# Optimization experiments

Measured on AMD Instinct MI355X. Metric: run time of the kernel, lower is better.

The kernel has to match this reference:

```python
import jax, jax.numpy as jnp
import numpy as np
from jax import lax

NPOINTS = [1024, 256, 64, 16]
RADII = [0.02, 0.04, 0.06, 0.08]
NSAMPLE = [32, 32, 16, 16]
# per-level MLP widths; first entry already includes the +3 for use_xyz concat
MLPS = [[6, 32, 32, 64], [67, 64, 64, 128], [131, 128, 128, 256], [259, 256, 256, 512]]
EPS = 1e-5


def setup_inputs() -> dict:
    key = jax.random.key(0)
    B, N = 8, 16384
    pc = jax.random.uniform(jax.random.fold_in(key, 0), (B, N, 6), jnp.float32)
    # xyz into a 0.2-cube so the hard-coded radii (0.02..0.08) find real neighborhoods
    pc = pc.at[..., :3].multiply(0.2)
    inp = {"pointcloud": pc}
    ki = 1
    for l, m in enumerate(MLPS):
        for j in range(len(m) - 1):
            cin, cout = m[j], m[j + 1]
            inp[f"w{l}{j}"] = jax.random.normal(jax.random.fold_in(key, ki), (cin, cout), jnp.float32) * (1.0 / float(np.sqrt(cin)))
            inp[f"g{l}{j}"] = jnp.ones((cout,), jnp.float32)
            inp[f"b{l}{j}"] = jnp.zeros((cout,), jnp.float32)
            ki += 1
    return inp


def _fps(xyz, npoint):
    # iterative farthest point sampling, start at index 0 (matches CUDA kernel)
    B, N, _ = xyz.shape

    def step(carry, _):
        mind, last = carry
        lastp = jnp.take_along_axis(xyz, last[:, None, None], axis=1)  # [B,1,3]
        d = jnp.sum((xyz - lastp) ** 2, axis=-1)                       # [B,N]
        mind = jnp.minimum(mind, d)
        nxt = jnp.argmax(mind, axis=1).astype(jnp.int32)
        return (mind, nxt), last

    init = (jnp.full((B, N), 1e10, xyz.dtype), jnp.zeros((B,), jnp.int32))
    _, idx = lax.scan(step, init, None, length=npoint)
    return jnp.transpose(idx)  # [B,npoint]


def _gather(pts, idx):
    # pts [B,N,C], idx [B,...] -> [B,...,C]
    return jax.vmap(lambda p, i: p[i])(pts, idx)


def _ball_query(xyz, centers, radius, nsample):
    # first nsample points (in index order) within radius; pad with first hit (0 if none)
    N = xyz.shape[1]
    d2 = jnp.sum((centers[:, :, None, :] - xyz[:, None, :, :]) ** 2, axis=-1)  # [B,S,N]
    key = jnp.where(d2 < radius * radius, jnp.arange(N, dtype=jnp.int32), N)
    negtop, _ = lax.top_k(-key, nsample)
    sel = -negtop                      # ascending candidate indices
    valid = sel < N
    first = jnp.where(valid[..., :1], sel[..., :1], 0)
    return jnp.where(valid, sel, first)  # [B,S,nsample] int32


def _sa(xyz, feats, npoint, radius, nsample, layers):
    fps_idx = lax.stop_gradient(_fps(xyz, npoint))
    new_xyz = _gather(xyz, fps_idx)                    # [B,S,3]
    idx = _ball_query(xyz, new_xyz, radius, nsample)   # [B,S,K]
    g = _gather(xyz, idx) - new_xyz[:, :, None, :]     # centered grouped xyz [B,S,K,3]
    g = jnp.concatenate([g, _gather(feats, idx)], axis=-1)  # use_xyz concat -> [B,S,K,3+C]
    x = g
    for W, gamma, beta in layers:
        x = jnp.einsum('bski,io->bsko', x, W)          # 1x1 conv, bias=False (bn on)
        mu = jnp.mean(x, axis=(0, 1, 2))               # BN training-mode batch stats
        var = jnp.var(x, axis=(0, 1, 2))
        x = jax.nn.relu(gamma * (x - mu) * lax.rsqrt(var + EPS) + beta)
    return new_xyz, jnp.max(x, axis=2)                 # max-pool over neighbors -> [B,S,Cout]


def reference(pointcloud, w00, g00, b00, w01, g01, b01, w02, g02, b02,
              w10, g10, b10, w11, g11, b11, w12, g12, b12,
              w20, g20, b20, w21, g21, b21, w22, g22, b22,
              w30, g30, b30, w31, g31, b31, w32, g32, b32):
    params = [
        [(w00, g00, b00), (w01, g01, b01), (w02, g02, b02)],
        [(w10, g10, b10), (w11, g11, b11), (w12, g12, b12)],
        [(w20, g20, b20), (w21, g21, b21), (w22, g22, b22)],
        [(w30, g30, b30), (w31, g31, b31), (w32, g32, b32)],
    ]
    xyz = pointcloud[..., :3]
    feats = pointcloud[..., 3:]   # channels-last (torch keeps [B,C,N]; pure layout diff)
    l_xyz, l_feats = [xyz], [feats]
    for k in range(4):
        nx, nf = _sa(l_xyz[k], l_feats[k], NPOINTS[k], RADII[k], NSAMPLE[k], params[k])
        l_xyz.append(nx)
        l_feats.append(nf)
    return tuple(l_xyz) + tuple(l_feats)
```

## Files before the change

kernel.cpp:

```cpp
#include <hip/hip_runtime.h>

#define WAVE 64

__global__ __launch_bounds__(256) void split_kernel(const float* __restrict__ pc,
    float* __restrict__ xyz, float* __restrict__ feats, int total) {
  int t = blockIdx.x * blockDim.x + threadIdx.x;
  if (t >= total) return;
  const float* p = pc + (size_t)t * 6;
  xyz[t * 3 + 0] = p[0]; xyz[t * 3 + 1] = p[1]; xyz[t * 3 + 2] = p[2];
  feats[t * 3 + 0] = p[3]; feats[t * 3 + 1] = p[4]; feats[t * 3 + 2] = p[5];
}

__global__ __launch_bounds__(256) void zero_kernel(float* __restrict__ p, int n) {
  int t = blockIdx.x * blockDim.x + threadIdx.x;
  if (t < n) p[t] = 0.f;
}

__device__ __forceinline__ float dpp_max_f32(float v) {
#define DPP_STEP_F(ctrl) { int t_ = __builtin_amdgcn_update_dpp( \
      __float_as_int(v), __float_as_int(v), ctrl, 0xf, 0xf, false); \
    v = fmaxf(v, __int_as_float(t_)); }
  DPP_STEP_F(0x111) DPP_STEP_F(0x112) DPP_STEP_F(0x114)
  DPP_STEP_F(0x118) DPP_STEP_F(0x142) DPP_STEP_F(0x143)
#undef DPP_STEP_F
  return v;
}
__device__ __forceinline__ unsigned dpp_max_u32(unsigned v) {
#define DPP_STEP_U(ctrl) { unsigned t_ = (unsigned)__builtin_amdgcn_update_dpp( \
      (int)v, (int)v, ctrl, 0xf, 0xf, false); \
    v = (t_ > v) ? t_ : v; }
  DPP_STEP_U(0x111) DPP_STEP_U(0x112) DPP_STEP_U(0x114)
  DPP_STEP_U(0x118) DPP_STEP_U(0x142) DPP_STEP_U(0x143)
#undef DPP_STEP_U
  return v;
}
__device__ __forceinline__ unsigned bcast63(unsigned v) {
  return (unsigned)__builtin_amdgcn_readlane((int)v, 63);
}

__global__ __launch_bounds__(1024, 4) void fps_big_kernel(const float* __restrict__ xyz,
    float* __restrict__ new_xyz, int N, int S) {
  const int b = blockIdx.x;
  const int tid = threadIdx.x;
  const int lane = tid & 63;
  const float* px = xyz + (size_t)b * N * 3;
  __shared__ unsigned long long s_key[3];
  float rx[16], ry[16], rz[16], mind[16];
#pragma unroll
  for (int p = 0; p < 16; ++p) {
    int i = tid + p * 1024;
    rx[p] = px[i * 3 + 0]; ry[p] = px[i * 3 + 1]; rz[p] = px[i * 3 + 2];
    asm volatile("" : "+v"(rx[p]), "+v"(ry[p]), "+v"(rz[p]));
    mind[p] = 1e10f;
  }
  if (tid < 3) s_key[tid] = 0ull;
  float qx = px[0], qy = px[1], qz = px[2];
  if (tid == 0) {
    float* o = new_xyz + (size_t)b * S * 3;
    o[0] = qx; o[1] = qy; o[2] = qz;
  }
  __syncthreads();
  for (unsigned it = 1; it < (unsigned)S; ++it) {
    float bestv = -1.f; unsigned besti = 0;
#pragma unroll
    for (int p = 0; p < 16; ++p) {
      float dx = __fsub_rn(rx[p], qx);
      float dy = __fsub_rn(ry[p], qy);
      float dz = __fsub_rn(rz[p], qz);
      float d = __fadd_rn(__fadd_rn(__fmul_rn(dx, dx), __fmul_rn(dy, dy)), __fmul_rn(dz, dz));
      float mo = fminf(mind[p], d);
      mind[p] = mo;
      if (mo > bestv) { bestv = mo; besti = (unsigned)(tid + p * 1024); }
    }
    float wm = dpp_max_f32(bestv);
    unsigned wmb = bcast63(__float_as_uint(wm));
    unsigned cand = (__float_as_uint(bestv) == wmb) ? (0xFFFFFFFFu - besti) : 0u;
    unsigned winv = bcast63(dpp_max_u32(cand));
    if (lane == 0) atomicMax(&s_key[it % 3u], ((unsigned long long)wmb << 32) | winv);
    if (tid == 0) s_key[(it + 1) % 3u] = 0ull;
    __syncthreads();
    unsigned long long k = s_key[it % 3u];
    int last = (int)(0xFFFFFFFFu - (unsigned)k);
    const float* q = px + (size_t)last * 3;
    qx = q[0]; qy = q[1]; qz = q[2];
    if (tid == 0) {
      float* o = new_xyz + ((size_t)b * S + it) * 3;
      o[0] = qx; o[1] = qy; o[2] = qz;
    }
  }
}

__global__ void fps_small_kernel(const float* __restrict__ xyz,
    float* __restrict__ new_xyz, int N, int S) {
  const int b = blockIdx.x;
  const int tid = threadIdx.x;
  const int lane = tid & 63;
  const float* px = xyz + (size_t)b * N * 3;
  __shared__ float sx[1024], sy[1024], sz[1024];
  __shared__ unsigned long long s_key[3];
  float x = px[tid * 3 + 0], y = px[tid * 3 + 1], z = px[tid * 3 + 2];
  sx[tid] = x; sy[tid] = y; sz[tid] = z;
  if (tid < 3) s_key[tid] = 0ull;
  float mind = 1e10f;
  float qx = px[0], qy = px[1], qz = px[2];
  if (tid == 0) {
    float* o = new_xyz + (size_t)b * S * 3;
    o[0] = qx; o[1] = qy; o[2] = qz;
  }
  __syncthreads();
  for (unsigned it = 1; it < (unsigned)S; ++it) {
    float dx = __fsub_rn(x, qx);
    float dy = __fsub_rn(y, qy);
    float dz = __fsub_rn(z, qz);
    float d = __fadd_rn(__fadd_rn(__fmul_rn(dx, dx), __fmul_rn(dy, dy)), __fmul_rn(dz, dz));
    mind = fminf(mind, d);
    float wm = dpp_max_f32(mind);
    unsigned wmb = bcast63(__float_as_uint(wm));
    unsigned cand = (__float_as_uint(mind) == wmb) ? (0xFFFFFFFFu - (unsigned)tid) : 0u;
    unsigned winv = bcast63(dpp_max_u32(cand));
    if (lane == 0) atomicMax(&s_key[it % 3u], ((unsigned long long)wmb << 32) | winv);
    if (tid == 0) s_key[(it + 1) % 3u] = 0ull;
    __syncthreads();
    unsigned long long k = s_key[it % 3u];
    int last = (int)(0xFFFFFFFFu - (unsigned)k);
    qx = sx[last]; qy = sy[last]; qz = sz[last];
    if (tid == 0) {
      float* o = new_xyz + ((size_t)b * S + it) * 3;
      o[0] = qx; o[1] = qy; o[2] = qz;
    }
  }
}

__global__ __launch_bounds__(256) void ballquery_kernel(const float* __restrict__ xyz,
    const float* __restrict__ centers, int* __restrict__ out_idx,
    int N, int S, int nsample, float r2) {
  int gw = (blockIdx.x * blockDim.x + threadIdx.x) >> 6;
  int lane = threadIdx.x & 63;
  int b = gw / S;
  int s = gw - b * S;
  const float* px = xyz + (size_t)b * N * 3;
  const float* cp = centers + ((size_t)b * S + s) * 3;
  float cx = cp[0], cy = cp[1], cz = cp[2];
  int* out = out_idx + ((size_t)b * S + s) * nsample;
  int cnt = 0;
  int firsti = 0;
  for (int base = 0; base < N; base += WAVE) {
    int i = base + lane;
    float dx = __fsub_rn(cx, px[i * 3 + 0]);
    float dy = __fsub_rn(cy, px[i * 3 + 1]);
    float dz = __fsub_rn(cz, px[i * 3 + 2]);
    float d = __fadd_rn(__fadd_rn(__fmul_rn(dx, dx), __fmul_rn(dy, dy)), __fmul_rn(dz, dz));
    bool hit = d < r2;
    unsigned long long m = __ballot(hit);
    if (hit) {
      int slot = cnt + __popcll(m & ((1ull << lane) - 1ull));
      if (slot < nsample) out[slot] = i;
    }
    if (cnt == 0 && m) firsti = base + __ffsll((unsigned long long)m) - 1;
    cnt += __popcll(m);
    if (cnt >= nsample) break;
  }
  for (int q = cnt + lane; q < nsample; q += WAVE) out[q] = firsti;
}

__global__ __launch_bounds__(256) void group_kernel(const float* __restrict__ xyz,
    const float* __restrict__ feats, const float* __restrict__ centers,
    const int* __restrict__ idx, float* __restrict__ X,
    int N, int S, int K, int ci, int R) {
  int t = blockIdx.x * blockDim.x + threadIdx.x;
  int C0 = ci + 3;
  int r = t / C0;
  if (r >= R) return;
  int c = t - r * C0;
  int g = r / K;
  int b = g / S;
  int j = idx[r];
  float v;
  if (c < 3) v = __fsub_rn(xyz[((size_t)b * N + j) * 3 + c], centers[(size_t)g * 3 + c]);
  else       v = feats[((size_t)b * N + j) * ci + (c - 3)];
  X[(size_t)r * C0 + c] = v;
}

#define BM 64
#define BN 64
#define BK 16
__global__ __launch_bounds__(256) void mm_fused_kernel(const float* __restrict__ A,
    const float* __restrict__ W, float* __restrict__ Y,
    float* __restrict__ st_out, const float* __restrict__ st_in,
    const float* __restrict__ g_in, const float* __restrict__ b_in,
    int R, int C, int Co, float inv_n) {
  __shared__ float As[BK][BM + 4];
  __shared__ float Bs[BK][BN + 4];
  __shared__ float s_mu[260], s_rs[260], s_g[260], s_b[260];
  __shared__ float s_sum[BN], s_sq[BN];
  int r0 = blockIdx.x * BM;
  int n0 = blockIdx.y * BN;
  int tid = threadIdx.x;
  int tx = tid & 15, ty = tid >> 4;
  if (st_in) {
    for (int c = tid; c < C; c += 256) {
      float mu = st_in[c] * inv_n;
      float var = st_in[512 + c] * inv_n - mu * mu;
      s_mu[c] = mu; s_rs[c] = rsqrtf(var + 1e-5f);
      s_g[c] = g_in[c]; s_b[c] = b_in[c];
    }
  }
  if (tid < BN) { s_sum[tid] = 0.f; s_sq[tid] = 0.f; }
  __syncthreads();
  float acc[4][4] = {};
  for (int k0 = 0; k0 < C; k0 += BK) {
#pragma unroll
    for (int u = 0; u < 4; ++u) {
      int lin = tid + u * 256;
      int row = lin >> 4;
      int cc = lin & 15;
      int c = k0 + cc;
      float v = 0.f;
      if (c < C) {
        v = A[(size_t)(r0 + row) * C + c];
        if (st_in) {
          v = s_g[c] * ((v - s_mu[c]) * s_rs[c]) + s_b[c];
          v = v > 0.f ? v : 0.f;
        }
      }
      As[cc][row] = v;
    }
#pragma unroll
    for (int u = 0; u < 4; ++u) {
      int lin = tid + u * 256;
      int kk = lin >> 6;
      int n = lin & 63;
      int c = k0 + kk;
      Bs[kk][n] = (c < C && (n0 + n) < Co) ? W[(size_t)c * Co + n0 + n] : 0.f;
    }
    __syncthreads();
#pragma unroll
    for (int kk = 0; kk < BK; ++kk) {
      float a0[4], b0[4];
#pragma unroll
      for (int i = 0; i < 4; ++i) a0[i] = As[kk][ty * 4 + i];
#pragma unroll
      for (int jj = 0; jj < 4; ++jj) b0[jj] = Bs[kk][tx * 4 + jj];
#pragma unroll
      for (int i = 0; i < 4; ++i)
#pragma unroll
        for (int jj = 0; jj < 4; ++jj)
          acc[i][jj] = fmaf(a0[i], b0[jj], acc[i][jj]);
    }
    __syncthreads();
  }
#pragma unroll
  for (int i = 0; i < 4; ++i) {
    int r = r0 + ty * 4 + i;
#pragma unroll
    for (int jj = 0; jj < 4; ++jj) {
      int n = n0 + tx * 4 + jj;
      if (n < Co) Y[(size_t)r * Co + n] = acc[i][jj];
    }
  }
#pragma unroll
  for (int jj = 0; jj < 4; ++jj) {
    float cs = 0.f, cq = 0.f;
#pragma unroll
    for (int i = 0; i < 4; ++i) { float v = acc[i][jj]; cs += v; cq += v * v; }
    atomicAdd(&s_sum[tx * 4 + jj], cs);
    atomicAdd(&s_sq[tx * 4 + jj], cq);
  }
  __syncthreads();
  if (tid < BN) {
    int n = n0 + tid;
    if (n < Co) {
      atomicAdd(&st_out[n], s_sum[tid]);
      atomicAdd(&st_out[512 + n], s_sq[tid]);
    }
  }
}

__global__ __launch_bounds__(256) void norm_relu_max_kernel(const float* __restrict__ Y,
    float* __restrict__ O, const float* __restrict__ st,
    const float* __restrict__ gamma, const float* __restrict__ beta,
    int G, int K, int Co, float inv_n) {
  int t = blockIdx.x * blockDim.x + threadIdx.x;
  if (t >= G * Co) return;
  int c = t & (Co - 1);
  int g = t / Co;
  float mu = st[c] * inv_n;
  float var = st[512 + c] * inv_n - mu * mu;
  float rs = rsqrtf(var + 1e-5f);
  float ga = gamma[c], be = beta[c];
  const float* yp = Y + (size_t)g * K * Co + c;
  float m = -1e30f;
  for (int k = 0; k < K; ++k) {
    float v = ga * ((yp[(size_t)k * Co] - mu) * rs) + be;
    m = fmaxf(m, v);
  }
  O[t] = m > 0.f ? m : 0.f;
}

extern "C" void kernel_launch(void* const* d_in, const int* in_sizes, int n_in,
                              void* d_out, int out_size, void* d_ws, size_t ws_size,
                              hipStream_t stream) {
  const float* pc = (const float*)d_in[0];
  float* out = (float*)d_out;
  char* wsb = (char*)d_ws;

  int* ballidx = (int*)wsb;
  float* stats = (float*)(wsb + ((size_t)1 << 20));
  float* bufA = (float*)(wsb + ((size_t)3 << 20));
  float* bufB = (float*)(wsb + ((size_t)37 << 20));

  const int B = 8;
  static const int Ns[4] = {16384, 1024, 256, 64};
  static const int Ss[4] = {1024, 256, 64, 16};
  static const int Ks[4] = {32, 32, 16, 16};
  static const double Rr[4] = {0.02, 0.04, 0.06, 0.08};
  static const int Ci[4] = {3, 64, 128, 256};
  static const int mlp[4][4] = {{6,32,32,64},{67,64,64,128},{131,128,128,256},{259,256,256,512}};
  static const size_t ox[5] = {0, 393216, 417792, 423936, 425472};
  static const size_t of[5] = {425856, 819072, 1343360, 1605504, 1736576};

  split_kernel<<<(B * 16384 + 255) / 256, 256, 0, stream>>>(pc, out + ox[0], out + of[0], B * 16384);
  zero_kernel<<<(12 * 1024 + 255) / 256, 256, 0, stream>>>(stats, 12 * 1024);

  for (int l = 0; l < 4; ++l) {
    const float* xyz = out + ox[l];
    const float* fts = out + of[l];
    float* nxyz = out + ox[l + 1];
    const int N = Ns[l], S = Ss[l], K = Ks[l], ci = Ci[l], C0 = ci + 3;
    const float r2 = (float)(Rr[l] * Rr[l]);

    if (l == 0) fps_big_kernel<<<B, 1024, 0, stream>>>(xyz, nxyz, N, S);
    else        fps_small_kernel<<<B, N, 0, stream>>>(xyz, nxyz, N, S);

    ballquery_kernel<<<(B * S) / 4, 256, 0, stream>>>(xyz, nxyz, ballidx, N, S, K, r2);

    const int R = B * S * K;
    {
      int total = R * C0;
      group_kernel<<<(total + 255) / 256, 256, 0, stream>>>(xyz, fts, nxyz, ballidx, bufA,
                                                            N, S, K, ci, R);
    }

    const float inv_n = 1.0f / (float)R;
    float* X = bufA; float* Y = bufB;
    const float* prev_st = nullptr;
    const float* prev_g = nullptr;
    const float* prev_b = nullptr;
    for (int j = 0; j < 3; ++j) {
      const int cin = mlp[l][j], cout = mlp[l][j + 1];
      const float* Wt = (const float*)d_in[1 + (l * 3 + j) * 3 + 0];
      const float* Ga = (const float*)d_in[1 + (l * 3 + j) * 3 + 1];
      const float* Be = (const float*)d_in[1 + (l * 3 + j) * 3 + 2];
      float* st = stats + (size_t)(l * 3 + j) * 1024;
      dim3 grid(R / 64, (cout + 63) / 64);
      mm_fused_kernel<<<grid, 256, 0, stream>>>(X, Wt, Y, st, prev_st, prev_g, prev_b,
                                                R, cin, cout, inv_n);
      if (j < 2) {
        prev_st = st; prev_g = Ga; prev_b = Be;
        float* tswap = X; X = Y; Y = tswap;
      } else {
        int G = B * S;
        int tot = G * cout;
        norm_relu_max_kernel<<<(tot + 255) / 256, 256, 0, stream>>>(Y, out + of[l + 1], st, Ga, Be,
                                                                    G, K, cout, inv_n);
      }
    }
  }
}
```

Baseline: 2.788 ms.

## Split level-0 farthest point sampling across eight cooperating blocks per batch

The single-block-per-batch FPS for the 16384-point level is replaced by eight blocks per batch, each owning a 2048-point chunk. Every iteration, each block publishes its local argmax key to a global slot array and spins on the other blocks' slots, with a timeout fallback. The aim is to cut the serial per-iteration distance work and raise GPU occupancy, at the cost of a cross-block global-memory handshake on every one of the 1024 iterations. The zero kernel is widened so it also clears the new slot region in the workspace. Correctness relies on all 64 blocks being co-resident.

```diff
diff --git a/kernel.cpp b/kernel.cpp
--- a/kernel.cpp
+++ b/kernel.cpp
@@ -38,39 +38,47 @@
   return (unsigned)__builtin_amdgcn_readlane((int)v, 63);
 }
 
-__global__ __launch_bounds__(1024, 4) void fps_big_kernel(const float* __restrict__ xyz,
-    float* __restrict__ new_xyz, int N, int S) {
-  const int b = blockIdx.x;
+#define FPS_W   8
+#define FPS_CH  2048
+#define FPS_PT  2
+__global__ __launch_bounds__(1024, 4) void fps_big_multi_kernel(
+    const float* __restrict__ xyz, float* __restrict__ new_xyz,
+    unsigned long long* __restrict__ gkey, int N, int S) {
+  const int b = blockIdx.x & 7;
+  const int w = blockIdx.x >> 3;
   const int tid = threadIdx.x;
   const int lane = tid & 63;
   const float* px = xyz + (size_t)b * N * 3;
+  const int base = w * FPS_CH;
   __shared__ unsigned long long s_key[3];
-  float rx[16], ry[16], rz[16], mind[16];
-#pragma unroll
-  for (int p = 0; p < 16; ++p) {
-    int i = tid + p * 1024;
+  __shared__ unsigned long long s_win;
+  float rx[FPS_PT], ry[FPS_PT], rz[FPS_PT], mind[FPS_PT];
+#pragma unroll
+  for (int p = 0; p < FPS_PT; ++p) {
+    int i = base + tid + p * 1024;
     rx[p] = px[i * 3 + 0]; ry[p] = px[i * 3 + 1]; rz[p] = px[i * 3 + 2];
     asm volatile("" : "+v"(rx[p]), "+v"(ry[p]), "+v"(rz[p]));
     mind[p] = 1e10f;
   }
   if (tid < 3) s_key[tid] = 0ull;
   float qx = px[0], qy = px[1], qz = px[2];
-  if (tid == 0) {
+  if (w == 0 && tid == 0) {
     float* o = new_xyz + (size_t)b * S * 3;
     o[0] = qx; o[1] = qy; o[2] = qz;
   }
   __syncthreads();
+  unsigned long long* slots = gkey + (size_t)b * S * FPS_W;
   for (unsigned it = 1; it < (unsigned)S; ++it) {
     float bestv = -1.f; unsigned besti = 0;
 #pragma unroll
-    for (int p = 0; p < 16; ++p) {
+    for (int p = 0; p < FPS_PT; ++p) {
       float dx = __fsub_rn(rx[p], qx);
       float dy = __fsub_rn(ry[p], qy);
       float dz = __fsub_rn(rz[p], qz);
       float d = __fadd_rn(__fadd_rn(__fmul_rn(dx, dx), __fmul_rn(dy, dy)), __fmul_rn(dz, dz));
       float mo = fminf(mind[p], d);
       mind[p] = mo;
-      if (mo > bestv) { bestv = mo; besti = (unsigned)(tid + p * 1024); }
+      if (mo > bestv) { bestv = mo; besti = (unsigned)(base + tid + p * 1024); }
     }
     float wm = dpp_max_f32(bestv);
     unsigned wmb = bcast63(__float_as_uint(wm));
@@ -79,11 +87,39 @@
     if (lane == 0) atomicMax(&s_key[it % 3u], ((unsigned long long)wmb << 32) | winv);
     if (tid == 0) s_key[(it + 1) % 3u] = 0ull;
     __syncthreads();
-    unsigned long long k = s_key[it % 3u];
-    int last = (int)(0xFFFFFFFFu - (unsigned)k);
+    if (tid < 64) {
+      unsigned long long k = 0ull;
+      if (lane == 0) {
+        atomicExch(&slots[(size_t)it * FPS_W + w], s_key[it % 3u]);
+      }
+      if (lane < FPS_W) {
+        unsigned long long* sl = &slots[(size_t)it * FPS_W + lane];
+        unsigned long long t0 = __builtin_amdgcn_s_memrealtime();
+        for (;;) {
+          k = __hip_atomic_load(sl, __ATOMIC_RELAXED, __HIP_MEMORY_SCOPE_AGENT);
+          if (k) break;
+          k = atomicMax(sl, 0ull);
+          if (k) break;
+          if (__builtin_amdgcn_s_memrealtime() - t0 > 2000000ull) {
+            k = 0xFFFFFFFFull;
+            break;
+          }
+          __builtin_amdgcn_s_sleep(2);
+        }
+      }
+#pragma unroll
+      for (int off = 1; off < FPS_W; off <<= 1) {
+        unsigned long long o = __shfl_xor(k, off, FPS_W);
+        if (o > k) k = o;
+      }
+      if (lane == 0) s_win = k;
+    }
+    __syncthreads();
+    unsigned long long k = s_win;
+    int last = (int)((0xFFFFFFFFu - (unsigned)k) & 16383u);
     const float* q = px + (size_t)last * 3;
     qx = q[0]; qy = q[1]; qz = q[2];
-    if (tid == 0) {
+    if (w == 0 && tid == 0) {
       float* o = new_xyz + ((size_t)b * S + it) * 3;
       o[0] = qx; o[1] = qy; o[2] = qz;
     }
@@ -306,6 +342,7 @@
 
   int* ballidx = (int*)wsb;
   float* stats = (float*)(wsb + ((size_t)1 << 20));
+  unsigned long long* gkey = (unsigned long long*)(wsb + ((size_t)2 << 20));
   float* bufA = (float*)(wsb + ((size_t)3 << 20));
   float* bufB = (float*)(wsb + ((size_t)37 << 20));
 
@@ -320,7 +357,7 @@
   static const size_t of[5] = {425856, 819072, 1343360, 1605504, 1736576};
 
   split_kernel<<<(B * 16384 + 255) / 256, 256, 0, stream>>>(pc, out + ox[0], out + of[0], B * 16384);
-  zero_kernel<<<(12 * 1024 + 255) / 256, 256, 0, stream>>>(stats, 12 * 1024);
+  zero_kernel<<<(524288 + 255) / 256, 256, 0, stream>>>(stats, 524288);
 
   for (int l = 0; l < 4; ++l) {
     const float* xyz = out + ox[l];
@@ -329,7 +366,7 @@
     const int N = Ns[l], S = Ss[l], K = Ks[l], ci = Ci[l], C0 = ci + 3;
     const float r2 = (float)(Rr[l] * Rr[l]);
 
-    if (l == 0) fps_big_kernel<<<B, 1024, 0, stream>>>(xyz, nxyz, N, S);
+    if (l == 0) fps_big_multi_kernel<<<B * FPS_W, 1024, 0, stream>>>(xyz, nxyz, gkey, N, S);
     else        fps_small_kernel<<<B, N, 0, stream>>>(xyz, nxyz, N, S);
 
     ballquery_kernel<<<(B * S) / 4, 256, 0, stream>>>(xyz, nxyz, ballidx, N, S, K, r2);
```

Result: faster. 2.491 ms (-10.7%).
